# Performance work log

Measured on AMD Instinct MI355X. Metric: run time of the kernel, lower is better.

## Reference

```python
import jax, jax.numpy as jnp
import numpy as np

# ---- problem constants (match init_kwargs / input_specs) ----
N = 10000        # atoms
E = 160000       # edges
G = 16           # graphs in batch
Z = 10           # num_elements
K = 64           # channels (count of 0e in hidden_irreps)
NB = 8           # num_bessel
SH = 9           # (max_ell+1)^2, max_ell=2
HID = 16         # MLP_irreps 16x0e
R_MAX = 5.0
AVG_NEI = 16.0
P = 5            # num_polynomial_cutoff
L_SLICES = ((0, 1, 0), (1, 4, 1), (4, 9, 2))  # (start, end, l) per irrep block


def _sph(u):
    # real spherical harmonics, 'component' normalization, lmax=2 -> 9 comps
    x, y, z = u[:, 0], u[:, 1], u[:, 2]
    s3, s15, s5 = 3.0 ** 0.5, 15.0 ** 0.5, 5.0 ** 0.5
    one = jnp.ones_like(x)
    return jnp.stack([one,
                      s3 * x, s3 * y, s3 * z,
                      s15 * x * y, s15 * y * z,
                      0.5 * s5 * (3.0 * z * z - 1.0),
                      s15 * x * z, 0.5 * s15 * (x * x - y * y)], axis=-1)


def _radial(r):
    # Bessel basis * polynomial cutoff (p=5)
    n = jnp.arange(1, NB + 1, dtype=r.dtype)
    bess = (2.0 / R_MAX) ** 0.5 * jnp.sin(n[None, :] * jnp.pi * r[:, None] / R_MAX) / r[:, None]
    xx = r / R_MAX
    f = (1.0 - 0.5 * (P + 1) * (P + 2) * xx ** P + P * (P + 2) * xx ** (P + 1)
         - 0.5 * P * (P + 1) * xx ** (P + 2)) * (xx < 1.0)
    return bess * f[:, None]


def _total_energy(positions, node_attrs, shifts, atomic_energies, W_embed, W_up,
                  R1, R2, R3, R4, W_out, W_sc, theta, W_mix, w_read0, Wr1, Wr2,
                  edge_index, batch):
    sender, receiver = edge_index[0], edge_index[1]
    vec = positions[receiver] - positions[sender] + shifts          # [E,3]
    r = jnp.sqrt(jnp.sum(vec * vec, axis=-1) + 1e-9)                # [E]
    u = vec / r[:, None]
    sh = _sph(u)                                                     # [E,9]
    edge_feats = _radial(r)                                          # [E,NB]

    node_e0 = node_attrs @ atomic_energies                           # [N]
    energies = jax.ops.segment_sum(node_e0, batch, num_segments=G)   # [G]

    feats = node_attrs @ W_embed                                     # [N,K] scalar feats
    for i in range(2):
        h = feats @ W_up[i]                                          # [N,K]
        xw = jax.nn.silu(edge_feats @ R1[i])
        xw = jax.nn.silu(xw @ R2[i])
        xw = jax.nn.silu(xw @ R3[i])
        rw = xw @ R4[i]                                              # [E,K] TP weights
        # channel-wise tensor product message + scatter to receiver
        m = rw[:, :, None] * h[sender][:, :, None] * sh[:, None, :]  # [E,K,9]
        A = jax.ops.segment_sum(m, receiver, num_segments=N) / AVG_NEI  # [N,K,9]
        A = jnp.concatenate([jnp.einsum('nkc,kj->njc', A[:, :, s:e], W_out[i, l])
                             for (s, e, l) in L_SLICES], axis=-1)    # per-l linear
        sc = jnp.einsum('nk,nz,zkj->nj', feats, node_attrs, W_sc[i])  # residual (0e)
        # symmetric-contraction product block (correlation=3), element-dependent
        a0 = A[:, :, 0]
        w = jnp.einsum('nz,pzk->pnk', node_attrs, theta[i])           # [3,N,K]
        B = (w[0] + w[1] * a0 + w[2] * a0 * a0)[:, :, None] * A      # [N,K,9]
        B = jnp.einsum('nkc,kj->njc', B, W_mix[i])
        B = B.at[:, :, 0].add(sc)
        feats = B[:, :, 0]                                            # invariant part
        if i == 0:
            node_e = feats @ w_read0                                  # linear readout
        else:
            node_e = jax.nn.silu(feats @ Wr1) @ Wr2                   # nonlinear readout
        energies = energies + jax.ops.segment_sum(node_e, batch, num_segments=G)
    return energies                                                   # [G]


def setup_inputs() -> dict:
    key = jax.random.key(0)
    ks = jax.random.split(key, 24)
    positions = jax.random.normal(ks[0], (N, 3), jnp.float32) * 1.5
    elems = jax.random.randint(ks[1], (N,), 0, Z)
    node_attrs = jax.nn.one_hot(elems, Z, dtype=jnp.float32)
    edge_index = jax.random.randint(ks[2], (2, E), 0, N)
    batch = jnp.sort(jax.random.randint(ks[3], (N,), 0, G))
    shifts = jnp.zeros((E, 3), jnp.float32)
    rn = lambda k, sh, s: jax.random.normal(k, sh, jnp.float32) * s
    return {
        'positions': positions, 'node_attrs': node_attrs, 'shifts': shifts,
        'atomic_energies': rn(ks[4], (Z,), 1.0),
        'W_embed': rn(ks[5], (Z, K), Z ** -0.5),
        'W_up': rn(ks[6], (2, K, K), K ** -0.5),
        'R1': rn(ks[7], (2, NB, 64), NB ** -0.5),
        'R2': rn(ks[8], (2, 64, 64), 64 ** -0.5),
        'R3': rn(ks[9], (2, 64, 64), 64 ** -0.5),
        'R4': rn(ks[10], (2, 64, K), 64 ** -0.5),
        'W_out': rn(ks[11], (2, 3, K, K), K ** -0.5),
        'W_sc': rn(ks[12], (2, Z, K, K), (Z * K) ** -0.5),
        'theta': rn(ks[13], (2, 3, Z, K), 0.1),
        'W_mix': rn(ks[14], (2, K, K), K ** -0.5),
        'w_read0': rn(ks[15], (K,), K ** -0.5),
        'Wr1': rn(ks[16], (K, HID), K ** -0.5),
        'Wr2': rn(ks[17], (HID,), HID ** -0.5),
        'edge_index': edge_index, 'batch': batch,
    }


def reference(positions, node_attrs, shifts, atomic_energies, W_embed, W_up,
              R1, R2, R3, R4, W_out, W_sc, theta, W_mix, w_read0, Wr1, Wr2,
              edge_index, batch):
    def energy(pos):
        return _total_energy(pos, node_attrs, shifts, atomic_energies, W_embed, W_up,
                             R1, R2, R3, R4, W_out, W_sc, theta, W_mix,
                             w_read0, Wr1, Wr2, edge_index, batch)
    total_energy, vjp_fn = jax.vjp(energy, positions)
    (g_pos,) = vjp_fn(jnp.ones((G,), positions.dtype))
    forces = -g_pos
    return total_energy, forces
```

## Files before the change

kernel.cpp:

```cpp
#include <hip/hip_runtime.h>
#include <math.h>

#define N_NODES 10000
#define N_EDGES 160000
#define G_SEG 16
#define ZDIM 10
#define KDIM 64
#define NBESS 8
#define HIDR 16
#define RMAXF 5.0f
#define AVG_NEI_F 16.0f
#define TBINS 256
#define ZROW (TBINS+1)

__device__ __forceinline__ float siluf(float x){ float s = 1.0f/(1.0f+expf(-x)); return x*s; }
__device__ __forceinline__ float dsiluf(float x){ float s = 1.0f/(1.0f+expf(-x)); return s*(1.0f + x*(1.0f-s)); }

__device__ __forceinline__ float waveReduce(float v){
  for (int off = 32; off > 0; off >>= 1) v += __shfl_down(v, off);
  return v;
}

__device__ __forceinline__ float rlane(float v, int l){
  return __int_as_float(__builtin_amdgcn_readlane(__float_as_int(v), l));
}

#define GATHER_NODE(NODE, PTR, PACK, IDXEXPR, LOADH, OUT) { \
  int beg_ = PTR[NODE]; int deg_ = PTR[(NODE)+1] - beg_; \
  float a0_=0.f,a1_=0.f,a2_=0.f,a3_=0.f; \
  for (int base_=0; base_<deg_; base_+=64){ \
    int m_ = min(64, deg_-base_); \
    int b_l = ZROW; float f_l = 0.f; int ix_l = 0; \
    if (lane < m_){ \
      int4 pk = PACK[beg_+base_+lane]; \
      float tp_ = __int_as_float(pk.x) * (TBINS/RMAXF); \
      b_l = (int)tp_; f_l = tp_ - (float)b_l; ix_l = IDXEXPR; \
    } \
    int mr_ = (m_ + 7) & ~7; \
    for (int i_=0; i_<mr_; i_+=8){ \
      int b0_=__shfl(b_l,i_),   b1_=__shfl(b_l,i_+1), b2_=__shfl(b_l,i_+2), b3_=__shfl(b_l,i_+3); \
      int b4_=__shfl(b_l,i_+4), b5_=__shfl(b_l,i_+5), b6_=__shfl(b_l,i_+6), b7_=__shfl(b_l,i_+7); \
      float f0_=__shfl(f_l,i_),   f1_=__shfl(f_l,i_+1), f2_=__shfl(f_l,i_+2), f3_=__shfl(f_l,i_+3); \
      float f4_=__shfl(f_l,i_+4), f5_=__shfl(f_l,i_+5), f6_=__shfl(f_l,i_+6), f7_=__shfl(f_l,i_+7); \
      int s0_=__shfl(ix_l,i_),   s1_=__shfl(ix_l,i_+1), s2_=__shfl(ix_l,i_+2), s3_=__shfl(ix_l,i_+3); \
      int s4_=__shfl(ix_l,i_+4), s5_=__shfl(ix_l,i_+5), s6_=__shfl(ix_l,i_+6), s7_=__shfl(ix_l,i_+7); \
      float2 F0_=Ft2[b0_*KDIM+lane]; float h0_=LOADH(s0_); \
      float2 F1_=Ft2[b1_*KDIM+lane]; float h1_=LOADH(s1_); \
      float2 F2_=Ft2[b2_*KDIM+lane]; float h2_=LOADH(s2_); \
      float2 F3_=Ft2[b3_*KDIM+lane]; float h3_=LOADH(s3_); \
      float2 F4_=Ft2[b4_*KDIM+lane]; float h4_=LOADH(s4_); \
      float2 F5_=Ft2[b5_*KDIM+lane]; float h5_=LOADH(s5_); \
      float2 F6_=Ft2[b6_*KDIM+lane]; float h6_=LOADH(s6_); \
      float2 F7_=Ft2[b7_*KDIM+lane]; float h7_=LOADH(s7_); \
      a0_ += (F0_.x + f0_*(F0_.y-F0_.x))*h0_; a1_ += (F1_.x + f1_*(F1_.y-F1_.x))*h1_; \
      a2_ += (F2_.x + f2_*(F2_.y-F2_.x))*h2_; a3_ += (F3_.x + f3_*(F3_.y-F3_.x))*h3_; \
      a0_ += (F4_.x + f4_*(F4_.y-F4_.x))*h4_; a1_ += (F5_.x + f5_*(F5_.y-F5_.x))*h5_; \
      a2_ += (F6_.x + f6_*(F6_.y-F6_.x))*h6_; a3_ += (F7_.x + f7_*(F7_.y-F7_.x))*h7_; \
    } } \
  OUT = ((a0_+a1_)+(a2_+a3_)); }

#define COOPMV(INV, W, OUTV) { \
  lds_in[w][lane] = INV; \
  __syncthreads(); \
  { float p0_=0.f,p1_=0.f,p2_=0.f,p3__=0.f; \
    const float* Wb_ = (W) + (w*16)*KDIM + lane; \
    _Pragma("unroll") \
    for (int kq_=0; kq_<4; kq_++){ \
      float4 x0_ = *(const float4*)&lds_in[0][w*16+4*kq_]; \
      float4 x1_ = *(const float4*)&lds_in[1][w*16+4*kq_]; \
      float4 x2_ = *(const float4*)&lds_in[2][w*16+4*kq_]; \
      float4 x3_ = *(const float4*)&lds_in[3][w*16+4*kq_]; \
      float w0_ = Wb_[(4*kq_+0)*KDIM]; \
      float w1_ = Wb_[(4*kq_+1)*KDIM]; \
      float w2_ = Wb_[(4*kq_+2)*KDIM]; \
      float w3_ = Wb_[(4*kq_+3)*KDIM]; \
      p0_  += x0_.x*w0_ + x0_.y*w1_ + x0_.z*w2_ + x0_.w*w3_; \
      p1_  += x1_.x*w0_ + x1_.y*w1_ + x1_.z*w2_ + x1_.w*w3_; \
      p2_  += x2_.x*w0_ + x2_.y*w1_ + x2_.z*w2_ + x2_.w*w3_; \
      p3__ += x3_.x*w0_ + x3_.y*w1_ + x3_.z*w2_ + x3_.w*w3_; \
    } \
    lds_part[w][0][lane]=p0_; lds_part[w][1][lane]=p1_; \
    lds_part[w][2][lane]=p2_; lds_part[w][3][lane]=p3__; } \
  __syncthreads(); \
  OUTV = ((lds_part[0][w][lane]+lds_part[1][w][lane]) + \
          (lds_part[2][w][lane]+lds_part[3][w][lane])); }

#define MVTROW(XV, MT, ROW, OUT) { \
  const float4* Mr_ = (const float4*)((MT) + (ROW)*KDIM); \
  float m0a_=0.f,m1a_=0.f,m2a_=0.f,m3a_=0.f; \
  _Pragma("unroll") \
  for (int kq_=0; kq_<KDIM/4; kq_++){ \
    float4 mm_ = Mr_[kq_]; \
    m0a_ += rlane(XV,4*kq_+0)*mm_.x; \
    m1a_ += rlane(XV,4*kq_+1)*mm_.y; \
    m2a_ += rlane(XV,4*kq_+2)*mm_.z; \
    m3a_ += rlane(XV,4*kq_+3)*mm_.w; \
  } \
  OUT = (m0a_+m1a_)+(m2a_+m3a_); }
#define MVT(XV, MT, OUT) MVTROW(XV, MT, lane, OUT)

#define LOADH_PLAIN(S) rows[(S)*KDIM + lane]
#define LOADH_G2(S)    gAr2c[(S)*KDIM + lane].x

#define NTABW 514
#define SETUP_BASE 317
#define NSETUP (SETUP_BASE + (NTABW+3)/4)

__global__ __launch_bounds__(256) void k_setup(
    const float* We, const float* Wup, const float* Wsc,
    const float* Wout, const float* Wmix,
    const float* Wr1,
    const float* attrs, const float* aE,
    const float* R1g, const float* R2g, const float* R3g, const float* R4g,
    float* M0, float* Msc0,
    float* WoT0, float* WoT1, float* WmixT0, float* WupT1,
    float* P1T, float* QtabT, float* WscT1, float* Wr1T,
    float2* Ft2_0, float2* Ft2_1, float* dF4f,
    int* z_buf, float* e_node){
  int blk = blockIdx.x, tid = threadIdx.x;
  const float* Wmix1 = Wmix + KDIM*KDIM;
  const float* Wsc1  = Wsc + ZDIM*KDIM*KDIM;
  if (blk < 5){
    int idx = blk*256 + tid;
    if (idx < 1280){
      int which = idx >= 640;
      int t = which ? idx - 640 : idx;
      int z = t >> 6, j = t & 63;
      float acc = 0.f;
      if (!which){
        #pragma unroll 8
        for (int k = 0; k < KDIM; k++) acc += We[z*KDIM + k] * Wup[k*KDIM + j];
        M0[z*KDIM + j] = acc;
      } else {
        #pragma unroll 8
        for (int k = 0; k < KDIM; k++) acc += We[z*KDIM + k] * Wsc[(z*KDIM + k)*KDIM + j];
        Msc0[z*KDIM + j] = acc;
      }
    }
  } else if (blk < 69){
    int t = (blk-5)*256 + tid;
    int arr = t >> 12;
    int rem = t & 4095;
    int j = rem >> 6, k = rem & 63;
    float v; float* dst;
    switch(arr){
      case 0: v = Wout[k*KDIM + j];                 dst = WoT0;   break;
      case 1: v = Wout[3*KDIM*KDIM + k*KDIM + j];   dst = WoT1;   break;
      case 2: v = Wmix[k*KDIM + j];                 dst = WmixT0; break;
      default:v = Wup[KDIM*KDIM + k*KDIM + j];      dst = WupT1;  break;
    }
    dst[rem] = v;
  } else if (blk < 73){
    int t = (blk-69)*256 + tid;
    int h = t >> 6, k = t & 63;
    float acc = 0.f;
    #pragma unroll 8
    for (int j = 0; j < KDIM; j++) acc += Wr1[j*HIDR + h] * Wmix1[k*KDIM + j];
    P1T[k*HIDR + h] = acc;
  } else if (blk < 113){
    int t = (blk-73)*256 + tid;
    int z = t >> 10;
    int rem = t & 1023;
    int h = rem >> 6, k = rem & 63;
    float acc = 0.f;
    #pragma unroll 8
    for (int j = 0; j < KDIM; j++) acc += Wr1[j*HIDR + h] * Wsc1[(z*KDIM + k)*KDIM + j];
    QtabT[(z*KDIM + k)*HIDR + h] = acc;
  } else if (blk < 153){
    int n = (blk-113)*256 + tid;
    if (n < N_NODES){
      int z = 0;
      for (int i = 1; i < ZDIM; i++) if (attrs[n*ZDIM+i] > 0.5f) z = i;
      z_buf[n] = z;
      e_node[n] = aE[z];
    }
  } else if (blk < 313){
    int t = (blk-153)*256 + tid;
    int zz = t >> 12; int rem = t & 4095;
    int j = rem >> 6, k = rem & 63;
    WscT1[(zz*KDIM + j)*KDIM + k] = Wsc1[(zz*KDIM + k)*KDIM + j];
  } else if (blk < SETUP_BASE){
    int t = (blk-313)*256 + tid;
    int h = t >> 6, j = t & 63;
    Wr1T[h*KDIM + j] = Wr1[j*HIDR + h];
  } else {
    int w = tid >> 6, j = tid & 63;
    int wave_id = (blk - SETUP_BASE)*4 + w;
    if (wave_id >= NTABW) return;
    int i = wave_id / (TBINS+1);
    int t = wave_id % (TBINS+1);
    float efv = 0.f, defv = 0.f;
    {
      double r = (double)t * (double)RMAXF / (double)TBINS;
      double wfr = (double)(j+1) * M_PI / (double)RMAXF;
      double c = sqrt(2.0 / (double)RMAXF);
      double bess, dbess;
      if (r < 1e-12){ bess = c*wfr; dbess = 0.0; }
      else {
        double sw = sin(wfr*r), cw = cos(wfr*r);
        bess = c*sw/r;
        dbess = c*(wfr*cw*r - sw)/(r*r);
      }
      double xx = r / (double)RMAXF;
      double f = 0.0, df = 0.0;
      if (xx < 1.0){
        double x2 = xx*xx, x4 = x2*x2, x5 = x4*xx, x6 = x5*xx, x7 = x6*xx;
        f = 1.0 - 21.0*x5 + 35.0*x6 - 15.0*x7;
        df = (-105.0*x4 + 210.0*x5 - 105.0*x6) / (double)RMAXF;
      }
      efv  = (float)(bess*f);
      defv = (float)(dbess*f + bess*df);
    }
    const float* R1 = R1g + i*NBESS*KDIM;
    const float* R2 = R2g + i*KDIM*KDIM;
    const float* R3 = R3g + i*KDIM*KDIM;
    const float* R4 = R4g + i*KDIM*KDIM;
    float z = 0.f, dz = 0.f;
    #pragma unroll
    for (int b = 0; b < NBESS; b++){
      float ef = __shfl(efv, b), def = __shfl(defv, b);
      float wv = R1[b*KDIM+j];
      z += ef*wv; dz += def*wv;
    }
    float v = siluf(z), dv = dsiluf(z)*dz;
    z = 0.f; dz = 0.f;
    for (int k = 0; k < KDIM; k++){
      float xv = __shfl(v, k), dxv = __shfl(dv, k);
      float wv = R2[k*KDIM+j];
      z += xv*wv; dz += dxv*wv;
    }
    float v2 = siluf(z), dv2 = dsiluf(z)*dz;
    z = 0.f; dz = 0.f;
    for (int k = 0; k < KDIM; k++){
      float xv = __shfl(v2, k), dxv = __shfl(dv2, k);
      float wv = R3[k*KDIM+j];
      z += xv*wv; dz += dxv*wv;
    }
    float v3 = siluf(z), dv3 = dsiluf(z)*dz;
    z = 0.f; dz = 0.f;
    for (int k = 0; k < KDIM; k++){
      float xv = __shfl(v3, k), dxv = __shfl(dv3, k);
      float wv = R4[k*KDIM+j];
      z += xv*wv; dz += dxv*wv;
    }
    float2* Ft = i ? Ft2_1 : Ft2_0;
    Ft[t*KDIM+j].x = z;  if (t > 0) Ft[(t-1)*KDIM+j].y = z;
    dF4f[(t*KDIM+j)*4 + 2*i] = dz;
    if (t > 0) dF4f[((t-1)*KDIM+j)*4 + 2*i + 1] = dz;
    if (t == 0) Ft[ZROW*KDIM + j] = make_float2(0.f, 0.f);
  }
}

__global__ __launch_bounds__(256) void k_edge_setup(const float* pos, const float* shifts, const int* ei,
                                                    const int* z_buf,
                                                    float4* evec, int4* emeta,
                                                    int* cnt_r, int* cnt_s){
  int e = blockIdx.x*256 + threadIdx.x;
  int s = ei[e], rcv = ei[N_EDGES + e];
  float dx = pos[rcv*3+0] - pos[s*3+0] + shifts[e*3+0];
  float dy = pos[rcv*3+1] - pos[s*3+1] + shifts[e*3+1];
  float dz = pos[rcv*3+2] - pos[s*3+2] + shifts[e*3+2];
  float r = sqrtf(dx*dx + dy*dy + dz*dz + 1e-9f);
  evec[e] = make_float4(dx, dy, dz, r);
  emeta[e] = make_int4(__float_as_int(r), s, rcv, z_buf[s]);
  if (r < RMAXF){
    atomicAdd(&cnt_s[s], 1);
    atomicAdd(&cnt_r[rcv], 1);
  }
}

__global__ __launch_bounds__(1024) void k_scan(const int* cnt_r, int* ptr_r, int* cur_r,
                                               const int* cnt_s, int* ptr_s, int* cur_s){
  __shared__ int wtot[16];
  __shared__ int woff[16];
  int tid = threadIdx.x;
  int w = tid >> 6, lane = tid & 63;
  const int* cnt = blockIdx.x ? cnt_s : cnt_r;
  int* ptr = blockIdx.x ? ptr_s : ptr_r;
  int* cur = blockIdx.x ? cur_s : cur_r;
  const int per = 10;
  int start = tid*per;
  int csum = 0;
  int cl[per];
  #pragma unroll
  for (int t = 0; t < per; t++){
    int i = start + t;
    int c = (i < N_NODES) ? cnt[i] : 0;
    cl[t] = c; csum += c;
  }
  int v = csum;
  #pragma unroll
  for (int off = 1; off < 64; off <<= 1){
    int u = __shfl_up(v, off);
    if (lane >= off) v += u;
  }
  if (lane == 63) wtot[w] = v;
  __syncthreads();
  if (w == 0 && lane < 16){
    int t = wtot[lane];
    int sv = t;
    #pragma unroll
    for (int off = 1; off < 16; off <<= 1){
      int u = __shfl_up(sv, off);
      if (lane >= off) sv += u;
    }
    woff[lane] = sv - t;
    if (lane == 15) ptr[N_NODES] = sv;
  }
  __syncthreads();
  int run = woff[w] + v - csum;
  #pragma unroll
  for (int t = 0; t < per; t++){
    int i = start + t;
    if (i < N_NODES){ ptr[i] = run; cur[i] = run; run += cl[t]; }
  }
}

__global__ __launch_bounds__(256) void k_fill(const int4* emeta, int* cur_r, int* cur_s,
                                              int4* pr_pack, int4* ps_pack){
  int e = blockIdx.x*256 + threadIdx.x;
  int4 m = emeta[e];
  float r = __int_as_float(m.x);
  if (r >= RMAXF) return;
  int p = atomicAdd(&cur_s[m.y], 1);
  ps_pack[p] = make_int4(m.x, m.z, e, 0);
  int p2 = atomicAdd(&cur_r[m.z], 1);
  pr_pack[p2] = make_int4(m.x, m.y, m.w, e);
}

__global__ __launch_bounds__(256) void k_layer0_fwd(
    const int* z_buf, const int* ptr_r, const int4* pr_pack,
    const float2* Ft2, const float* M0,
    const float* Wout0, const float* theta0, const float* Wmix0,
    const float* Msc0, const float* w_read0,
    const float* Wup1, const float* WscT1,
    float* A0_out, float* h1, float* sc1, float* e_node){
  __shared__ __align__(16) float lds_in[4][KDIM];
  __shared__ float lds_part[4][4][KDIM];
  int tid = threadIdx.x;
  int w = tid >> 6, lane = tid & 63;
  int node = blockIdx.x*4 + w;
  int z = z_buf[node];
  const float* rows = M0;
  float acc;
  GATHER_NODE(node, ptr_r, pr_pack, pk.z, LOADH_PLAIN, acc)
  acc *= (1.0f/AVG_NEI_F);
  float a0;
  COOPMV(acc, Wout0, a0)
  A0_out[node*KDIM+lane] = a0;
  float t0 = theta0[(0*ZDIM+z)*KDIM+lane];
  float t1 = theta0[(1*ZDIM+z)*KDIM+lane];
  float t2 = theta0[(2*ZDIM+z)*KDIM+lane];
  float v = (t0 + t1*a0 + t2*a0*a0)*a0;
  float f;
  COOPMV(v, Wmix0, f)
  f += Msc0[z*KDIM+lane];
  float p = waveReduce(f * w_read0[lane]);
  if (lane == 0) e_node[node] += p;
  float h;
  COOPMV(f, Wup1, h)
  h1[node*KDIM+lane] = h;
  float s;
  MVT(f, WscT1 + z*KDIM*KDIM, s)
  sc1[node*KDIM+lane] = s;
}

__global__ __launch_bounds__(256) void k_layer1_fwd_bwd(
    const int* z_buf, const int* ptr_r, const int4* pr_pack,
    const float2* Ft2, const float* h1rows,
    const float* Wout1, const float* theta1, const float* Wmix1,
    const float* sc1, const float* Wr1T, const float* Wr2,
    const float* P1T, const float* QtabT, const float* WoT1, const float* w_read0,
    float2* gAr2, float* gF1, float* e_node){
  __shared__ __align__(16) float lds_in[4][KDIM];
  __shared__ float lds_part[4][4][KDIM];
  int tid = threadIdx.x;
  int w = tid >> 6, lane = tid & 63;
  int node = blockIdx.x*4 + w;
  int z = z_buf[node];
  const float* rows = h1rows;
  float acc;
  GATHER_NODE(node, ptr_r, pr_pack, pk.y, LOADH_PLAIN, acc)
  acc *= (1.0f/AVG_NEI_F);
  float a0;
  COOPMV(acc, Wout1, a0)
  float t0 = theta1[(0*ZDIM+z)*KDIM+lane];
  float t1 = theta1[(1*ZDIM+z)*KDIM+lane];
  float t2 = theta1[(2*ZDIM+z)*KDIM+lane];
  float v = (t0 + t1*a0 + t2*a0*a0)*a0;
  float f;
  COOPMV(v, Wmix1, f)
  f += sc1[node*KDIM+lane];
  int hh = lane & 15;
  float tpart;
  MVTROW(f, Wr1T, hh, tpart)
  float wr2 = Wr2[hh];
  float ne = waveReduce(siluf(tpart)*wr2);
  if (lane == 0) e_node[node] += 0.25f*ne;
  float coeff = dsiluf(tpart)*wr2;
  float gP, gs;
  { const float4* Pp_ = (const float4*)(P1T + lane*HIDR);
    const float4* Qp_ = (const float4*)(QtabT + (z*KDIM + lane)*HIDR);
    float pa0_=0.f,pa1_=0.f,pa2_=0.f,pa3_=0.f, qa0_=0.f,qa1_=0.f,qa2_=0.f,qa3_=0.f;
    #pragma unroll
    for (int hq_=0; hq_<HIDR/4; hq_++){
      float4 pm_ = Pp_[hq_]; float4 qm_ = Qp_[hq_];
      float c0_=rlane(coeff,4*hq_+0), c1_=rlane(coeff,4*hq_+1);
      float c2_=rlane(coeff,4*hq_+2), c3_=rlane(coeff,4*hq_+3);
      pa0_ += c0_*pm_.x; pa1_ += c1_*pm_.y; pa2_ += c2_*pm_.z; pa3_ += c3_*pm_.w;
      qa0_ += c0_*qm_.x; qa1_ += c1_*qm_.y; qa2_ += c2_*qm_.z; qa3_ += c3_*qm_.w;
    }
    gP = (pa0_+pa1_)+(pa2_+pa3_); gs = (qa0_+qa1_)+(qa2_+qa3_);
  }
  gF1[node*KDIM+lane] = w_read0[lane] + gs;
  float u = t0 + 2.f*t1*a0 + 3.f*t2*a0*a0;
  float vl = gP*u;
  float gAr;
  COOPMV(vl, WoT1, gAr)
  gAr2[node*KDIM+lane].x = gAr * (1.0f/AVG_NEI_F);
}

__global__ __launch_bounds__(256) void k_energy(const float* e_node, const int* batch, float* out_e){
  __shared__ float part[G_SEG];
  int tid = threadIdx.x;
  if (tid < G_SEG) part[tid] = 0.f;
  __syncthreads();
  int n = blockIdx.x*256 + tid;
  if (n < N_NODES) atomicAdd(&part[batch[n]], e_node[n]);
  __syncthreads();
  if (tid < G_SEG) atomicAdd(&out_e[tid], part[tid]);
}

__global__ __launch_bounds__(256) void k_bwd_gH0(
    const int* z_buf, const int* ptr_s, const int4* ps_pack,
    const float2* Ft2, const float2* gAr2c, const float* WupT1, const float* gF1,
    const float* A00, const float* WmixT0, const float* WoT0, const float* theta0,
    float2* gAr2){
  __shared__ __align__(16) float lds_in[4][KDIM];
  __shared__ float lds_part[4][4][KDIM];
  int tid = threadIdx.x;
  int w = tid >> 6, lane = tid & 63;
  int node = blockIdx.x*4 + w;
  float ga;
  GATHER_NODE(node, ptr_s, ps_pack, pk.y, LOADH_G2, ga)
  float gfh;
  COOPMV(ga, WupT1, gfh)
  float gt = gF1[node*KDIM+lane] + gfh;
  float gP;
  COOPMV(gt, WmixT0, gP)
  int z = z_buf[node];
  float a = A00[node*KDIM+lane];
  float t0 = theta0[(0*ZDIM+z)*KDIM+lane];
  float t1 = theta0[(1*ZDIM+z)*KDIM+lane];
  float t2 = theta0[(2*ZDIM+z)*KDIM+lane];
  float u = t0 + 2.f*t1*a + 3.f*t2*a*a;
  float vl = gP*u;
  float gAr;
  COOPMV(vl, WoT0, gAr)
  gAr2[node*KDIM+lane].y = gAr * (1.0f/AVG_NEI_F);
}

__global__ __launch_bounds__(256) void k_gr(const int4* emeta, const float4* dF4,
                                            const float2* gAr2, const float* h1, const float* M0,
                                            float4* evec){
  int tid = threadIdx.x;
  int e = blockIdx.x*16 + (tid >> 4);
  int li = tid & 15;
  int4 m = emeta[e];
  float r = __int_as_float(m.x);
  if (r >= RMAXF) return;
  float tp = r * (TBINS / RMAXF);
  int b = (int)tp; if (b > TBINS-1) b = TBINS-1;
  float fr = tp - (float)b;
  int k0 = li*4;
  const float4* dp = dF4 + b*KDIM + k0;
  float4 d0 = dp[0], d1 = dp[1], d2 = dp[2], d3 = dp[3];
  const float4* gp = (const float4*)(gAr2 + m.z*KDIM + k0);
  float4 g01 = gp[0], g23 = gp[1];
  float4 hv = *(const float4*)(h1 + m.y*KDIM + k0);
  float4 mv = *(const float4*)(M0 + m.w*KDIM + k0);
  float v;
  v  = g01.x*hv.x*(d0.z + fr*(d0.w-d0.z)) + g01.y*mv.x*(d0.x + fr*(d0.y-d0.x));
  v += g01.z*hv.y*(d1.z + fr*(d1.w-d1.z)) + g01.w*mv.y*(d1.x + fr*(d1.y-d1.x));
  v += g23.x*hv.z*(d2.z + fr*(d2.w-d2.z)) + g23.y*mv.z*(d2.x + fr*(d2.y-d2.x));
  v += g23.z*hv.w*(d3.z + fr*(d3.w-d3.z)) + g23.w*mv.w*(d3.x + fr*(d3.y-d3.x));
  #pragma unroll
  for (int off = 8; off > 0; off >>= 1) v += __shfl_xor(v, off);
  if (li == 0) evec[e].w = v / r;
}

__global__ __launch_bounds__(256) void k_force(const int* ptr_r, const int4* pr_pack,
                                               const int* ptr_s, const int4* ps_pack,
                                               const float4* evec,
                                               float* out_f){
  int tid = threadIdx.x;
  int node = blockIdx.x*16 + (tid >> 4);
  int li = tid & 15;
  float fx=0.f, fy=0.f, fz=0.f;
  int beg = ptr_r[node], end = ptr_r[node+1];
  for (int idx = beg + li; idx < end; idx += 16){
    int e = pr_pack[idx].w;
    float4 ev = evec[e];
    fx -= ev.w*ev.x; fy -= ev.w*ev.y; fz -= ev.w*ev.z;
  }
  beg = ptr_s[node]; end = ptr_s[node+1];
  for (int idx = beg + li; idx < end; idx += 16){
    int e = ps_pack[idx].z;
    float4 ev = evec[e];
    fx += ev.w*ev.x; fy += ev.w*ev.y; fz += ev.w*ev.z;
  }
  #pragma unroll
  for (int off = 8; off > 0; off >>= 1){
    fx += __shfl_xor(fx, off);
    fy += __shfl_xor(fy, off);
    fz += __shfl_xor(fz, off);
  }
  if (li == 0){
    out_f[node*3+0] = fx; out_f[node*3+1] = fy; out_f[node*3+2] = fz;
  }
}

extern "C" void kernel_launch(void* const* d_in, const int* in_sizes, int n_in,
                              void* d_out, int out_size, void* d_ws, size_t ws_size,
                              hipStream_t stream){
  const float* pos    = (const float*)d_in[0];
  const float* attrs  = (const float*)d_in[1];
  const float* shifts = (const float*)d_in[2];
  const float* aE     = (const float*)d_in[3];
  const float* We     = (const float*)d_in[4];
  const float* Wup    = (const float*)d_in[5];
  const float* R1     = (const float*)d_in[6];
  const float* R2     = (const float*)d_in[7];
  const float* R3     = (const float*)d_in[8];
  const float* R4     = (const float*)d_in[9];
  const float* Wout   = (const float*)d_in[10];
  const float* Wsc    = (const float*)d_in[11];
  const float* theta  = (const float*)d_in[12];
  const float* Wmix   = (const float*)d_in[13];
  const float* w_read0= (const float*)d_in[14];
  const float* Wr1    = (const float*)d_in[15];
  const float* Wr2    = (const float*)d_in[16];
  const int*   ei     = (const int*)d_in[17];
  const int*   batch  = (const int*)d_in[18];

  char* base = (char*)d_ws;
  size_t off = 0;
  auto alloc = [&](size_t bytes)->void*{
    void* p = base + off;
    off = (off + bytes + 255) & ~(size_t)255;
    return p;
  };
  float4* evec   = (float4*)alloc(N_EDGES*sizeof(float4));
  int4*   emeta  = (int4*)alloc(N_EDGES*sizeof(int4));
  int4*   pr_pack= (int4*)alloc(N_EDGES*sizeof(int4));
  int4*   ps_pack= (int4*)alloc(N_EDGES*sizeof(int4));
  float*  e_node = (float*)alloc(N_NODES*sizeof(float));
  float*  h1     = (float*)alloc(N_NODES*KDIM*sizeof(float));
  float*  sc1    = (float*)alloc(N_NODES*KDIM*sizeof(float));
  float*  A00    = (float*)alloc(N_NODES*KDIM*sizeof(float));
  float*  gF1    = (float*)alloc(N_NODES*KDIM*sizeof(float));
  float2* gAr2   = (float2*)alloc(N_NODES*KDIM*sizeof(float2));
  float2* Ft2_0  = (float2*)alloc((TBINS+2)*KDIM*sizeof(float2));
  float2* Ft2_1  = (float2*)alloc((TBINS+2)*KDIM*sizeof(float2));
  float4* dF4    = (float4*)alloc((TBINS+1)*KDIM*sizeof(float4));
  float*  M0     = (float*)alloc(ZDIM*KDIM*sizeof(float));
  float*  Msc0   = (float*)alloc(ZDIM*KDIM*sizeof(float));
  float*  WoT0   = (float*)alloc(KDIM*KDIM*sizeof(float));
  float*  WoT1   = (float*)alloc(KDIM*KDIM*sizeof(float));
  float*  WmixT0 = (float*)alloc(KDIM*KDIM*sizeof(float));
  float*  WupT1  = (float*)alloc(KDIM*KDIM*sizeof(float));
  float*  P1T    = (float*)alloc(KDIM*HIDR*sizeof(float));
  float*  QtabT  = (float*)alloc(ZDIM*KDIM*HIDR*sizeof(float));
  float*  WscT1  = (float*)alloc(ZDIM*KDIM*KDIM*sizeof(float));
  float*  Wr1T   = (float*)alloc(HIDR*KDIM*sizeof(float));
  int* z_buf = (int*)alloc(N_NODES*sizeof(int));
  int* cnt_r = (int*)alloc(N_NODES*sizeof(int));
  int* cnt_s = (int*)alloc(N_NODES*sizeof(int));
  int* ptr_r = (int*)alloc((N_NODES+1)*sizeof(int));
  int* ptr_s = (int*)alloc((N_NODES+1)*sizeof(int));
  int* cur_r = (int*)alloc(N_NODES*sizeof(int));
  int* cur_s = (int*)alloc(N_NODES*sizeof(int));

  float* out_e = (float*)d_out;
  float* out_f = out_e + G_SEG;

  hipMemsetAsync(d_out, 0, (size_t)out_size*sizeof(float), stream);
  hipMemsetAsync(cnt_r, 0, N_NODES*sizeof(int), stream);
  hipMemsetAsync(cnt_s, 0, N_NODES*sizeof(int), stream);

  const int NB4 = N_NODES/4;
  const int EB  = N_EDGES/256;
  const int NBt = (N_NODES+255)/256;

  const float* Wup1 = Wup + KDIM*KDIM;
  const float* Wout1 = Wout + 3*KDIM*KDIM;
  const float* theta1 = theta + 3*ZDIM*KDIM;
  const float* Wmix1 = Wmix + KDIM*KDIM;

  k_setup<<<NSETUP,256,0,stream>>>(We, Wup, Wsc, Wout, Wmix, Wr1, attrs, aE,
                                   R1, R2, R3, R4,
                                   M0, Msc0, WoT0, WoT1, WmixT0, WupT1,
                                   P1T, QtabT, WscT1, Wr1T,
                                   Ft2_0, Ft2_1, (float*)dF4,
                                   z_buf, e_node);
  k_edge_setup<<<EB,256,0,stream>>>(pos, shifts, ei, z_buf, evec, emeta, cnt_r, cnt_s);
  k_scan<<<2,1024,0,stream>>>(cnt_r, ptr_r, cur_r, cnt_s, ptr_s, cur_s);
  k_fill<<<EB,256,0,stream>>>(emeta, cur_r, cur_s, pr_pack, ps_pack);

  k_layer0_fwd<<<NB4,256,0,stream>>>(z_buf, ptr_r, pr_pack, Ft2_0, M0,
      Wout, theta, Wmix, Msc0, w_read0, Wup1, WscT1,
      A00, h1, sc1, e_node);
  k_layer1_fwd_bwd<<<NB4,256,0,stream>>>(z_buf, ptr_r, pr_pack, Ft2_1, h1,
      Wout1, theta1, Wmix1, sc1, Wr1T, Wr2,
      P1T, QtabT, WoT1, w_read0,
      gAr2, gF1, e_node);
  k_energy<<<NBt,256,0,stream>>>(e_node, batch, out_e);

  k_bwd_gH0<<<NB4,256,0,stream>>>(z_buf, ptr_s, ps_pack, Ft2_1, gAr2, WupT1, gF1,
      A00, WmixT0, WoT0, theta, gAr2);
  k_gr<<<N_EDGES/16,256,0,stream>>>(emeta, dF4, gAr2, h1, M0, evec);
  k_force<<<N_NODES/16,256,0,stream>>>(ptr_r, pr_pack, ptr_s, ps_pack, evec, out_f);
}
```

Baseline: 270.3 us.

## Stage 64x64 weight matrices in LDS and use per-wave matvecs with 512-thread blocks

Replaces the cooperative four-wave matvec, which needed two barriers per product, with a per-wave matvec that reads a transposed weight matrix staged once into padded LDS and broadcasts inputs via readlane. Blocks grow to 512 threads (8 nodes) so each staging load is shared by more nodes. The energy segment-sum kernel is merged into the backward gH0 launch as extra blocks to save a launch. The cost is about 52 KB of LDS per block and a staging phase at block start, which may limit occupancy.

```diff
diff --git a/kernel.cpp b/kernel.cpp
--- a/kernel.cpp
+++ b/kernel.cpp
@@ -12,6 +12,7 @@
 #define AVG_NEI_F 16.0f
 #define TBINS 256
 #define ZROW (TBINS+1)
+#define LSTR 68
 
 __device__ __forceinline__ float siluf(float x){ float s = 1.0f/(1.0f+expf(-x)); return x*s; }
 __device__ __forceinline__ float dsiluf(float x){ float s = 1.0f/(1.0f+expf(-x)); return s*(1.0f + x*(1.0f-s)); }
@@ -59,31 +60,27 @@
     } } \
   OUT = ((a0_+a1_)+(a2_+a3_)); }
 
-#define COOPMV(INV, W, OUTV) { \
-  lds_in[w][lane] = INV; \
-  __syncthreads(); \
-  { float p0_=0.f,p1_=0.f,p2_=0.f,p3__=0.f; \
-    const float* Wb_ = (W) + (w*16)*KDIM + lane; \
-    _Pragma("unroll") \
-    for (int kq_=0; kq_<4; kq_++){ \
-      float4 x0_ = *(const float4*)&lds_in[0][w*16+4*kq_]; \
-      float4 x1_ = *(const float4*)&lds_in[1][w*16+4*kq_]; \
-      float4 x2_ = *(const float4*)&lds_in[2][w*16+4*kq_]; \
-      float4 x3_ = *(const float4*)&lds_in[3][w*16+4*kq_]; \
-      float w0_ = Wb_[(4*kq_+0)*KDIM]; \
-      float w1_ = Wb_[(4*kq_+1)*KDIM]; \
-      float w2_ = Wb_[(4*kq_+2)*KDIM]; \
-      float w3_ = Wb_[(4*kq_+3)*KDIM]; \
-      p0_  += x0_.x*w0_ + x0_.y*w1_ + x0_.z*w2_ + x0_.w*w3_; \
-      p1_  += x1_.x*w0_ + x1_.y*w1_ + x1_.z*w2_ + x1_.w*w3_; \
-      p2_  += x2_.x*w0_ + x2_.y*w1_ + x2_.z*w2_ + x2_.w*w3_; \
-      p3__ += x3_.x*w0_ + x3_.y*w1_ + x3_.z*w2_ + x3_.w*w3_; \
-    } \
-    lds_part[w][0][lane]=p0_; lds_part[w][1][lane]=p1_; \
-    lds_part[w][2][lane]=p2_; lds_part[w][3][lane]=p3__; } \
-  __syncthreads(); \
-  OUTV = ((lds_part[0][w][lane]+lds_part[1][w][lane]) + \
-          (lds_part[2][w][lane]+lds_part[3][w][lane])); }
+#define STAGE3(W0P, W1P, W2P) { \
+  for (int idx_ = tid; idx_ < KDIM*KDIM; idx_ += 512){ \
+    int r_ = idx_ >> 6, c_ = idx_ & 63; \
+    smW[0][r_*LSTR + c_] = (W0P)[idx_]; \
+    smW[1][r_*LSTR + c_] = (W1P)[idx_]; \
+    smW[2][r_*LSTR + c_] = (W2P)[idx_]; \
+  } \
+  __syncthreads(); }
+
+#define MVLDS(XV, M, OUT) { \
+  const float* Lr_ = &smW[M][lane*LSTR]; \
+  float m0_=0.f,m1_=0.f,m2_=0.f,m3_=0.f; \
+  _Pragma("unroll") \
+  for (int kq_=0; kq_<KDIM/4; kq_++){ \
+    float4 mm_ = *(const float4*)&Lr_[4*kq_]; \
+    m0_ += rlane(XV,4*kq_+0)*mm_.x; \
+    m1_ += rlane(XV,4*kq_+1)*mm_.y; \
+    m2_ += rlane(XV,4*kq_+2)*mm_.z; \
+    m3_ += rlane(XV,4*kq_+3)*mm_.w; \
+  } \
+  OUT = (m0_+m1_)+(m2_+m3_); }
 
 #define MVTROW(XV, MT, ROW, OUT) { \
   const float4* Mr_ = (const float4*)((MT) + (ROW)*KDIM); \
@@ -103,7 +100,7 @@
 #define LOADH_G2(S)    gAr2c[(S)*KDIM + lane].x
 
 #define NTABW 514
-#define SETUP_BASE 317
+#define SETUP_BASE 333
 #define NSETUP (SETUP_BASE + (NTABW+3)/4)
 
 __global__ __launch_bounds__(256) void k_setup(
@@ -113,7 +110,7 @@
     const float* attrs, const float* aE,
     const float* R1g, const float* R2g, const float* R3g, const float* R4g,
     float* M0, float* Msc0,
-    float* WoT0, float* WoT1, float* WmixT0, float* WupT1,
+    float* WoT0, float* WoT1, float* WmixT0, float* WupT1, float* WmixT1,
     float* P1T, float* QtabT, float* WscT1, float* Wr1T,
     float2* Ft2_0, float2* Ft2_1, float* dF4f,
     int* z_buf, float* e_node){
@@ -137,7 +134,7 @@
         Msc0[z*KDIM + j] = acc;
       }
     }
-  } else if (blk < 69){
+  } else if (blk < 85){
     int t = (blk-5)*256 + tid;
     int arr = t >> 12;
     int rem = t & 4095;
@@ -147,18 +144,19 @@
       case 0: v = Wout[k*KDIM + j];                 dst = WoT0;   break;
       case 1: v = Wout[3*KDIM*KDIM + k*KDIM + j];   dst = WoT1;   break;
       case 2: v = Wmix[k*KDIM + j];                 dst = WmixT0; break;
-      default:v = Wup[KDIM*KDIM + k*KDIM + j];      dst = WupT1;  break;
+      case 3: v = Wup[KDIM*KDIM + k*KDIM + j];      dst = WupT1;  break;
+      default:v = Wmix[KDIM*KDIM + k*KDIM + j];     dst = WmixT1; break;
     }
     dst[rem] = v;
-  } else if (blk < 73){
-    int t = (blk-69)*256 + tid;
+  } else if (blk < 89){
+    int t = (blk-85)*256 + tid;
     int h = t >> 6, k = t & 63;
     float acc = 0.f;
     #pragma unroll 8
     for (int j = 0; j < KDIM; j++) acc += Wr1[j*HIDR + h] * Wmix1[k*KDIM + j];
     P1T[k*HIDR + h] = acc;
-  } else if (blk < 113){
-    int t = (blk-73)*256 + tid;
+  } else if (blk < 129){
+    int t = (blk-89)*256 + tid;
     int z = t >> 10;
     int rem = t & 1023;
     int h = rem >> 6, k = rem & 63;
@@ -166,21 +164,21 @@
     #pragma unroll 8
     for (int j = 0; j < KDIM; j++) acc += Wr1[j*HIDR + h] * Wsc1[(z*KDIM + k)*KDIM + j];
     QtabT[(z*KDIM + k)*HIDR + h] = acc;
-  } else if (blk < 153){
-    int n = (blk-113)*256 + tid;
+  } else if (blk < 169){
+    int n = (blk-129)*256 + tid;
     if (n < N_NODES){
       int z = 0;
       for (int i = 1; i < ZDIM; i++) if (attrs[n*ZDIM+i] > 0.5f) z = i;
       z_buf[n] = z;
       e_node[n] = aE[z];
     }
-  } else if (blk < 313){
-    int t = (blk-153)*256 + tid;
+  } else if (blk < 329){
+    int t = (blk-169)*256 + tid;
     int zz = t >> 12; int rem = t & 4095;
     int j = rem >> 6, k = rem & 63;
     WscT1[(zz*KDIM + j)*KDIM + k] = Wsc1[(zz*KDIM + k)*KDIM + j];
   } else if (blk < SETUP_BASE){
-    int t = (blk-313)*256 + tid;
+    int t = (blk-329)*256 + tid;
     int h = t >> 6, j = t & 63;
     Wr1T[h*KDIM + j] = Wr1[j*HIDR + h];
   } else {
@@ -328,68 +326,69 @@
   pr_pack[p2] = make_int4(m.x, m.y, m.w, e);
 }
 
-__global__ __launch_bounds__(256) void k_layer0_fwd(
+__global__ __launch_bounds__(512) void k_layer0_fwd(
     const int* z_buf, const int* ptr_r, const int4* pr_pack,
     const float2* Ft2, const float* M0,
-    const float* Wout0, const float* theta0, const float* Wmix0,
-    const float* Msc0, const float* w_read0,
-    const float* Wup1, const float* WscT1,
+    const float* WoT0, const float* WmixT0, const float* WupT1,
+    const float* theta0, const float* Msc0, const float* w_read0,
+    const float* WscT1,
     float* A0_out, float* h1, float* sc1, float* e_node){
-  __shared__ __align__(16) float lds_in[4][KDIM];
-  __shared__ float lds_part[4][4][KDIM];
+  __shared__ __align__(16) float smW[3][KDIM*LSTR];
   int tid = threadIdx.x;
   int w = tid >> 6, lane = tid & 63;
-  int node = blockIdx.x*4 + w;
+  STAGE3(WoT0, WmixT0, WupT1)
+  int node = blockIdx.x*8 + w;
   int z = z_buf[node];
   const float* rows = M0;
   float acc;
   GATHER_NODE(node, ptr_r, pr_pack, pk.z, LOADH_PLAIN, acc)
   acc *= (1.0f/AVG_NEI_F);
   float a0;
-  COOPMV(acc, Wout0, a0)
+  MVLDS(acc, 0, a0)
   A0_out[node*KDIM+lane] = a0;
   float t0 = theta0[(0*ZDIM+z)*KDIM+lane];
   float t1 = theta0[(1*ZDIM+z)*KDIM+lane];
   float t2 = theta0[(2*ZDIM+z)*KDIM+lane];
   float v = (t0 + t1*a0 + t2*a0*a0)*a0;
   float f;
-  COOPMV(v, Wmix0, f)
+  MVLDS(v, 1, f)
   f += Msc0[z*KDIM+lane];
   float p = waveReduce(f * w_read0[lane]);
   if (lane == 0) e_node[node] += p;
   float h;
-  COOPMV(f, Wup1, h)
+  MVLDS(f, 2, h)
   h1[node*KDIM+lane] = h;
   float s;
   MVT(f, WscT1 + z*KDIM*KDIM, s)
   sc1[node*KDIM+lane] = s;
 }
 
-__global__ __launch_bounds__(256) void k_layer1_fwd_bwd(
+__global__ __launch_bounds__(512) void k_layer1_fwd_bwd(
     const int* z_buf, const int* ptr_r, const int4* pr_pack,
     const float2* Ft2, const float* h1rows,
-    const float* Wout1, const float* theta1, const float* Wmix1,
+    const float* WoT1, const float* WmixT1, const float* Wout1raw,
+    const float* theta1,
     const float* sc1, const float* Wr1T, const float* Wr2,
-    const float* P1T, const float* QtabT, const float* WoT1, const float* w_read0,
+    const float* P1T, const float* QtabT, const float* w_read0,
     float2* gAr2, float* gF1, float* e_node){
-  __shared__ __align__(16) float lds_in[4][KDIM];
-  __shared__ float lds_part[4][4][KDIM];
+  __shared__ __align__(16) float smW[3][KDIM*LSTR];
   int tid = threadIdx.x;
   int w = tid >> 6, lane = tid & 63;
-  int node = blockIdx.x*4 + w;
+  STAGE3(WoT1, WmixT1, Wout1raw)
+  int node = blockIdx.x*8 + w;
   int z = z_buf[node];
   const float* rows = h1rows;
   float acc;
   GATHER_NODE(node, ptr_r, pr_pack, pk.y, LOADH_PLAIN, acc)
   acc *= (1.0f/AVG_NEI_F);
   float a0;
-  COOPMV(acc, Wout1, a0)
+  MVLDS(acc, 0, a0)
   float t0 = theta1[(0*ZDIM+z)*KDIM+lane];
   float t1 = theta1[(1*ZDIM+z)*KDIM+lane];
   float t2 = theta1[(2*ZDIM+z)*KDIM+lane];
   float v = (t0 + t1*a0 + t2*a0*a0)*a0;
   float f;
-  COOPMV(v, Wmix1, f)
+  MVLDS(v, 1, f)
   f += sc1[node*KDIM+lane];
   int hh = lane & 15;
   float tpart;
@@ -416,38 +415,43 @@
   float u = t0 + 2.f*t1*a0 + 3.f*t2*a0*a0;
   float vl = gP*u;
   float gAr;
-  COOPMV(vl, WoT1, gAr)
+  MVLDS(vl, 2, gAr)
   gAr2[node*KDIM+lane].x = gAr * (1.0f/AVG_NEI_F);
 }
 
-__global__ __launch_bounds__(256) void k_energy(const float* e_node, const int* batch, float* out_e){
-  __shared__ float part[G_SEG];
+#define NBWD_NODE (N_NODES/8)
+#define NBWD_EN   ((N_NODES+511)/512)
+
+__global__ __launch_bounds__(512) void k_bwd_gH0(
+    const int* z_buf, const int* ptr_s, const int4* ps_pack,
+    const float2* Ft2, const float2* gAr2c,
+    const float* Wup1raw, const float* Wmix0raw, const float* Wout0raw,
+    const float* gF1,
+    const float* A00, const float* theta0,
+    const float* e_node, const int* batch, float* out_e,
+    float2* gAr2){
   int tid = threadIdx.x;
-  if (tid < G_SEG) part[tid] = 0.f;
-  __syncthreads();
-  int n = blockIdx.x*256 + tid;
-  if (n < N_NODES) atomicAdd(&part[batch[n]], e_node[n]);
-  __syncthreads();
-  if (tid < G_SEG) atomicAdd(&out_e[tid], part[tid]);
-}
-
-__global__ __launch_bounds__(256) void k_bwd_gH0(
-    const int* z_buf, const int* ptr_s, const int4* ps_pack,
-    const float2* Ft2, const float2* gAr2c, const float* WupT1, const float* gF1,
-    const float* A00, const float* WmixT0, const float* WoT0, const float* theta0,
-    float2* gAr2){
-  __shared__ __align__(16) float lds_in[4][KDIM];
-  __shared__ float lds_part[4][4][KDIM];
-  int tid = threadIdx.x;
+  if (blockIdx.x >= NBWD_NODE){
+    __shared__ float part[G_SEG];
+    if (tid < G_SEG) part[tid] = 0.f;
+    __syncthreads();
+    int n = (blockIdx.x - NBWD_NODE)*512 + tid;
+    if (n < N_NODES) atomicAdd(&part[batch[n]], e_node[n]);
+    __syncthreads();
+    if (tid < G_SEG) atomicAdd(&out_e[tid], part[tid]);
+    return;
+  }
+  __shared__ __align__(16) float smW[3][KDIM*LSTR];
   int w = tid >> 6, lane = tid & 63;
-  int node = blockIdx.x*4 + w;
+  STAGE3(Wup1raw, Wmix0raw, Wout0raw)
+  int node = blockIdx.x*8 + w;
   float ga;
   GATHER_NODE(node, ptr_s, ps_pack, pk.y, LOADH_G2, ga)
   float gfh;
-  COOPMV(ga, WupT1, gfh)
+  MVLDS(ga, 0, gfh)
   float gt = gF1[node*KDIM+lane] + gfh;
   float gP;
-  COOPMV(gt, WmixT0, gP)
+  MVLDS(gt, 1, gP)
   int z = z_buf[node];
   float a = A00[node*KDIM+lane];
   float t0 = theta0[(0*ZDIM+z)*KDIM+lane];
@@ -456,7 +460,7 @@
   float u = t0 + 2.f*t1*a + 3.f*t2*a*a;
   float vl = gP*u;
   float gAr;
-  COOPMV(vl, WoT0, gAr)
+  MVLDS(vl, 2, gAr)
   gAr2[node*KDIM+lane].y = gAr * (1.0f/AVG_NEI_F);
 }
 
@@ -569,6 +573,7 @@
   float*  WoT1   = (float*)alloc(KDIM*KDIM*sizeof(float));
   float*  WmixT0 = (float*)alloc(KDIM*KDIM*sizeof(float));
   float*  WupT1  = (float*)alloc(KDIM*KDIM*sizeof(float));
+  float*  WmixT1 = (float*)alloc(KDIM*KDIM*sizeof(float));
   float*  P1T    = (float*)alloc(KDIM*HIDR*sizeof(float));
   float*  QtabT  = (float*)alloc(ZDIM*KDIM*HIDR*sizeof(float));
   float*  WscT1  = (float*)alloc(ZDIM*KDIM*KDIM*sizeof(float));
@@ -588,18 +593,16 @@
   hipMemsetAsync(cnt_r, 0, N_NODES*sizeof(int), stream);
   hipMemsetAsync(cnt_s, 0, N_NODES*sizeof(int), stream);
 
-  const int NB4 = N_NODES/4;
+  const int NB8 = N_NODES/8;
   const int EB  = N_EDGES/256;
-  const int NBt = (N_NODES+255)/256;
 
   const float* Wup1 = Wup + KDIM*KDIM;
   const float* Wout1 = Wout + 3*KDIM*KDIM;
   const float* theta1 = theta + 3*ZDIM*KDIM;
-  const float* Wmix1 = Wmix + KDIM*KDIM;
 
   k_setup<<<NSETUP,256,0,stream>>>(We, Wup, Wsc, Wout, Wmix, Wr1, attrs, aE,
                                    R1, R2, R3, R4,
-                                   M0, Msc0, WoT0, WoT1, WmixT0, WupT1,
+                                   M0, Msc0, WoT0, WoT1, WmixT0, WupT1, WmixT1,
                                    P1T, QtabT, WscT1, Wr1T,
                                    Ft2_0, Ft2_1, (float*)dF4,
                                    z_buf, e_node);
@@ -607,17 +610,17 @@
   k_scan<<<2,1024,0,stream>>>(cnt_r, ptr_r, cur_r, cnt_s, ptr_s, cur_s);
   k_fill<<<EB,256,0,stream>>>(emeta, cur_r, cur_s, pr_pack, ps_pack);
 
-  k_layer0_fwd<<<NB4,256,0,stream>>>(z_buf, ptr_r, pr_pack, Ft2_0, M0,
-      Wout, theta, Wmix, Msc0, w_read0, Wup1, WscT1,
+  k_layer0_fwd<<<NB8,512,0,stream>>>(z_buf, ptr_r, pr_pack, Ft2_0, M0,
+      WoT0, WmixT0, WupT1, theta, Msc0, w_read0, WscT1,
       A00, h1, sc1, e_node);
-  k_layer1_fwd_bwd<<<NB4,256,0,stream>>>(z_buf, ptr_r, pr_pack, Ft2_1, h1,
-      Wout1, theta1, Wmix1, sc1, Wr1T, Wr2,
-      P1T, QtabT, WoT1, w_read0,
+  k_layer1_fwd_bwd<<<NB8,512,0,stream>>>(z_buf, ptr_r, pr_pack, Ft2_1, h1,
+      WoT1, WmixT1, Wout1, theta1, sc1, Wr1T, Wr2,
+      P1T, QtabT, w_read0,
       gAr2, gF1, e_node);
-  k_energy<<<NBt,256,0,stream>>>(e_node, batch, out_e);
-
-  k_bwd_gH0<<<NB4,256,0,stream>>>(z_buf, ptr_s, ps_pack, Ft2_1, gAr2, WupT1, gF1,
-      A00, WmixT0, WoT0, theta, gAr2);
+
+  k_bwd_gH0<<<NBWD_NODE + NBWD_EN,512,0,stream>>>(z_buf, ptr_s, ps_pack, Ft2_1, gAr2,
+      Wup1, Wmix, Wout, gF1, A00, theta,
+      e_node, batch, out_e, gAr2);
   k_gr<<<N_EDGES/16,256,0,stream>>>(emeta, dF4, gAr2, h1, M0, evec);
   k_force<<<N_NODES/16,256,0,stream>>>(ptr_r, pr_pack, ptr_s, ps_pack, evec, out_f);
 }
```

Result: no change. 270.7 us (+0.2%).
